# Optimization experiments

Measured on AMD Instinct MI355X. Metric: run time of the kernel, lower is better.

## Reference

```python
import jax, jax.numpy as jnp
import numpy as np

VOCAB, DIM, B, S = 32000, 1024, 64, 512

def setup_inputs() -> dict:
    key = jax.random.key(0)
    ks = jax.random.split(key, 16)
    std = 1.0 / np.sqrt(DIM)
    return {
        "x": jax.random.randint(ks[0], (B,), 0, VOCAB),
        "h": jax.random.normal(ks[1], (B, DIM), jnp.float32),
        "c": jax.random.normal(ks[2], (B, DIM), jnp.float32),
        "enc_y": jax.random.normal(ks[3], (B, S, DIM), jnp.float32),
        "F_emb": jax.random.normal(ks[4], (VOCAB, DIM), jnp.float32),
        "W1_w": jax.random.uniform(ks[5], (DIM, DIM), jnp.float32, -std, std),
        "W1_b": jnp.zeros((DIM,), jnp.float32),
        "W2_w": jax.random.uniform(ks[6], (DIM, DIM), jnp.float32, -std, std),
        "W2_b": jnp.zeros((DIM,), jnp.float32),
        "V_w": jax.random.uniform(ks[7], (1, DIM), jnp.float32, -std, std),
        "V_b": jnp.zeros((1,), jnp.float32),
        "W_ih": jax.random.uniform(ks[8], (4 * DIM, DIM), jnp.float32, -std, std),
        "W_hh": jax.random.uniform(ks[9], (4 * DIM, DIM), jnp.float32, -std, std),
        "b_ih": jax.random.uniform(ks[10], (4 * DIM,), jnp.float32, -std, std),
        "b_hh": jax.random.uniform(ks[11], (4 * DIM,), jnp.float32, -std, std),
        "fc_w": jax.random.uniform(ks[12], (VOCAB, DIM), jnp.float32, -std, std),
        "fc_b": jnp.zeros((VOCAB,), jnp.float32),
    }

def reference(x, h, c, enc_y, F_emb, W1_w, W1_b, W2_w, W2_b, V_w, V_b,
              W_ih, W_hh, b_ih, b_hh, fc_w, fc_b):
    # Bahdanau additive attention (weights returned; context is dead code for layer=1)
    i_s = jnp.einsum('bsd,ed->bse', enc_y, W1_w) + W1_b          # [B,S,D]
    j_s = (h @ W2_w.T + W2_b)[:, None, :]                        # [B,1,D]
    score = jnp.tanh(i_s + j_s)                                  # [B,S,D]
    att = jax.nn.softmax(score @ V_w.T + V_b, axis=1)            # [B,S,1]
    # embedding lookup for the step token
    emb = F_emb[x]                                               # [B,D]
    # single-step LSTM (pytorch gate order: i, f, g, o)
    gates = emb @ W_ih.T + b_ih + h @ W_hh.T + b_hh              # [B,4D]
    ig, fg, gg, og = jnp.split(gates, 4, axis=-1)
    c_new = jax.nn.sigmoid(fg) * c + jax.nn.sigmoid(ig) * jnp.tanh(gg)
    h_new = jax.nn.sigmoid(og) * jnp.tanh(c_new)
    out = h_new + emb                                            # residual skip
    logits = out @ fc_w.T + fc_b                                 # [B,VOCAB]
    return logits, h_new, c_new, att
```

## Files before the change

### kernel.cpp

```cpp
#include <hip/hip_runtime.h>

#define DEV __device__ __forceinline__

typedef __bf16 bf16_t;
typedef bf16_t bf16x8 __attribute__((ext_vector_type(8)));
typedef float f32x4 __attribute__((ext_vector_type(4)));

static constexpr int VOCAB = 32000, DIM = 1024, BATCH = 64, SEQ = 512;
static constexpr int M_SC = BATCH * SEQ;

DEV unsigned short f2bf(float f) {
  unsigned u = __builtin_bit_cast(unsigned, f);
  u += 0x7FFFu + ((u >> 16) & 1u);
  return (unsigned short)(u >> 16);
}

DEV float sigmf(float x) {
  x = fminf(fmaxf(x, -30.f), 30.f);
  return 1.0f / (1.0f + __expf(-x));
}

DEV float tanh_fast(float x) {
  x = fminf(fmaxf(x, -20.f), 20.f);
  float e = __expf(2.0f * x);
  return (e - 1.0f) / (e + 1.0f);
}

DEV void gload_lds16(const void* g, void* l) {
  __builtin_amdgcn_global_load_lds(
      (__attribute__((address_space(1))) void*)(g),
      (__attribute__((address_space(3))) void*)(l), 16, 0, 0);
}

__global__ void __launch_bounds__(256) k_prep(const float* __restrict__ enc,
                                              const float* __restrict__ w1,
                                              unsigned short* __restrict__ enc_b,
                                              unsigned short* __restrict__ w1_b,
                                              float* __restrict__ att_l,
                                              const int* __restrict__ x,
                                              const float* __restrict__ Femb,
                                              const float* __restrict__ h,
                                              float* __restrict__ emb_f,
                                              unsigned short* __restrict__ eh_b,
                                              unsigned short* __restrict__ h_b) {
  if (blockIdx.x >= 1984) {
    int b = blockIdx.x - 1984;
    int tok = x[b];
    for (int d = threadIdx.x; d < DIM; d += 256) {
      float e = Femb[(size_t)tok * DIM + d];
      float hv = h[b * DIM + d];
      emb_f[b * DIM + d] = e;
      unsigned short eb = f2bf(e), hb = f2bf(hv);
      eh_b[b * 2 * DIM + d] = eb;
      eh_b[b * 2 * DIM + DIM + d] = hb;
      h_b[b * DIM + d] = hb;
    }
  }
  int gid = blockIdx.x * 256 + threadIdx.x;
  if (gid < M_SC) att_l[gid] = 0.f;
  const int ENC4 = (M_SC * DIM) / 4;
  const int TOT4 = ENC4 + (DIM * DIM) / 4;
  int stride = gridDim.x * 256;
  for (int i = gid; i < TOT4; i += stride) {
    float4 v;
    unsigned short* dst;
    if (i < ENC4) {
      v = ((const float4*)enc)[i];
      dst = enc_b + (size_t)i * 4;
    } else {
      v = ((const float4*)w1)[i - ENC4];
      dst = w1_b + (size_t)(i - ENC4) * 4;
    }
    ushort4 o;
    o.x = f2bf(v.x); o.y = f2bf(v.y); o.z = f2bf(v.z); o.w = f2bf(v.w);
    *(ushort4*)dst = o;
  }
}

__global__ void __launch_bounds__(256) k_skinny(
    const unsigned short* __restrict__ A, int lda,
    const float* __restrict__ B1, const float* __restrict__ B2, int ksplit,
    const float* __restrict__ bias, float* __restrict__ C, int N, int K) {
  __shared__ unsigned short As[2][64 * 128];
  __shared__ unsigned short Bs[2][16 * 128];
  int t = threadIdx.x;
  int l = t & 63, w = t >> 6;
  int n0 = blockIdx.x * 16;
  f32x4 acc = {};
  int rx = (l & 7) << 3;

  float4 vB[2];

  auto loadB = [&](int k0) {
    const float* Bsrc;
    int kk;
    if (k0 < ksplit) { Bsrc = B1; kk = k0; } else { Bsrc = B2; kk = k0 - ksplit; }
#pragma unroll
    for (int i = 0; i < 2; ++i) {
      int lin = i * 256 + t;
      int row = lin >> 5, c4 = (lin & 31) * 4;
      vB[i] = *(const float4*)(Bsrc + (size_t)(n0 + row) * 1024 + kk + c4);
    }
  };
  auto writeB = [&](int bufi) {
#pragma unroll
    for (int i = 0; i < 2; ++i) {
      int lin = i * 256 + t;
      int row = lin >> 5, c4 = (lin & 31) * 4;
      ushort4 o;
      o.x = f2bf(vB[i].x); o.y = f2bf(vB[i].y); o.z = f2bf(vB[i].z); o.w = f2bf(vB[i].w);
      *(ushort4*)&Bs[bufi][row * 128 + (c4 ^ ((row & 7) << 3))] = o;
    }
  };
  auto stageA = [&](int k0, int bufi) {
#pragma unroll
    for (int i = 0; i < 4; ++i) {
      int sbase = i * 256 + w * 64;
      int s = sbase + l;
      int row = s >> 4;
      int scol = ((s & 15) ^ (row & 7)) * 8;
      gload_lds16(A + (size_t)row * lda + k0 + scol, &As[bufi][sbase * 8]);
    }
  };
  auto compute = [&](int bufi) {
#pragma unroll
    for (int kf = 0; kf < 4; ++kf) {
      int ko = kf * 32 + 8 * (l >> 4);
      int ar = w * 16 + (l & 15);
      bf16x8 af = *(const bf16x8*)&As[bufi][ar * 128 + (ko ^ rx)];
      bf16x8 bf = *(const bf16x8*)&Bs[bufi][(l & 15) * 128 + (ko ^ rx)];
      acc = __builtin_amdgcn_mfma_f32_16x16x32_bf16(af, bf, acc, 0, 0, 0);
    }
  };

  loadB(0);
  stageA(0, 0);
  writeB(0);
  asm volatile("s_waitcnt lgkmcnt(0)" ::: "memory");

  int nk = K / 128;
  int cur = 0;
  for (int kt = 0; kt < nk - 1; ++kt) {
    loadB((kt + 1) * 128);
    stageA((kt + 1) * 128, cur ^ 1);
    asm volatile("s_waitcnt vmcnt(6)\n\ts_barrier" ::: "memory");
    compute(cur);
    writeB(cur ^ 1);
    asm volatile("s_waitcnt lgkmcnt(0)\n\ts_barrier" ::: "memory");
    cur ^= 1;
  }
  asm volatile("s_waitcnt vmcnt(0)\n\ts_barrier" ::: "memory");
  compute(cur);

  int cn = n0 + (l & 15);
  float bv = bias ? bias[cn] : 0.f;
#pragma unroll
  for (int r = 0; r < 4; ++r) {
    int m = w * 16 + (l >> 4) * 4 + r;
    C[(size_t)m * N + cn] = acc[r] + bv;
  }
}

__global__ void __launch_bounds__(256) k_skinny32(
    const unsigned short* __restrict__ A,
    const float* __restrict__ B, const float* __restrict__ bias,
    float* __restrict__ C, int N, int K) {
  __shared__ unsigned short As[2][64 * 128];
  __shared__ unsigned short Bs[2][32 * 128];
  int t = threadIdx.x;
  int l = t & 63, w = t >> 6;
  int n0 = blockIdx.x * 32;
  f32x4 acc0 = {}, acc1 = {};
  int rx = (l & 7) << 3;

  float4 vB[4];

  auto loadB = [&](int k0) {
#pragma unroll
    for (int i = 0; i < 4; ++i) {
      int lin = i * 256 + t;
      int row = lin >> 5, c4 = (lin & 31) * 4;
      vB[i] = *(const float4*)(B + (size_t)(n0 + row) * 1024 + k0 + c4);
    }
  };
  auto writeB = [&](int bufi) {
#pragma unroll
    for (int i = 0; i < 4; ++i) {
      int lin = i * 256 + t;
      int row = lin >> 5, c4 = (lin & 31) * 4;
      ushort4 o;
      o.x = f2bf(vB[i].x); o.y = f2bf(vB[i].y); o.z = f2bf(vB[i].z); o.w = f2bf(vB[i].w);
      *(ushort4*)&Bs[bufi][row * 128 + (c4 ^ ((row & 7) << 3))] = o;
    }
  };
  auto stageA = [&](int k0, int bufi) {
#pragma unroll
    for (int i = 0; i < 4; ++i) {
      int sbase = i * 256 + w * 64;
      int s = sbase + l;
      int row = s >> 4;
      int scol = ((s & 15) ^ (row & 7)) * 8;
      gload_lds16(A + (size_t)row * DIM + k0 + scol, &As[bufi][sbase * 8]);
    }
  };
  auto compute = [&](int bufi) {
#pragma unroll
    for (int kf = 0; kf < 4; ++kf) {
      int ko = kf * 32 + 8 * (l >> 4);
      int ar = w * 16 + (l & 15);
      bf16x8 af = *(const bf16x8*)&As[bufi][ar * 128 + (ko ^ rx)];
      bf16x8 b0 = *(const bf16x8*)&Bs[bufi][(l & 15) * 128 + (ko ^ rx)];
      bf16x8 b1 = *(const bf16x8*)&Bs[bufi][((l & 15) + 16) * 128 + (ko ^ rx)];
      acc0 = __builtin_amdgcn_mfma_f32_16x16x32_bf16(af, b0, acc0, 0, 0, 0);
      acc1 = __builtin_amdgcn_mfma_f32_16x16x32_bf16(af, b1, acc1, 0, 0, 0);
    }
  };

  loadB(0);
  stageA(0, 0);
  writeB(0);
  asm volatile("s_waitcnt lgkmcnt(0)" ::: "memory");

  int nk = K / 128;
  int cur = 0;
  for (int kt = 0; kt < nk - 1; ++kt) {
    loadB((kt + 1) * 128);
    stageA((kt + 1) * 128, cur ^ 1);
    asm volatile("s_waitcnt vmcnt(8)\n\ts_barrier" ::: "memory");
    compute(cur);
    writeB(cur ^ 1);
    asm volatile("s_waitcnt lgkmcnt(0)\n\ts_barrier" ::: "memory");
    cur ^= 1;
  }
  asm volatile("s_waitcnt vmcnt(0)\n\ts_barrier" ::: "memory");
  compute(cur);

  int cn = n0 + (l & 15);
  float bv0 = bias ? bias[cn] : 0.f;
  float bv1 = bias ? bias[cn + 16] : 0.f;
#pragma unroll
  for (int r = 0; r < 4; ++r) {
    int m = w * 16 + (l >> 4) * 4 + r;
    C[(size_t)m * N + cn] = acc0[r] + bv0;
    C[(size_t)m * N + cn + 16] = acc1[r] + bv1;
  }
}

#define READ_A(MH)                                                              \
  do {                                                                          \
    _Pragma("unroll") for (int mf = 0; mf < 4; ++mf)                            \
    _Pragma("unroll") for (int kk = 0; kk < 2; ++kk) {                          \
      int row_ = wm * 128 + (MH) * 64 + mf * 16 + lm;                           \
      fa[mf][kk] = *(const bf16x8*)&As[ct][row_ * 64 + ((kk * 32 + 8 * lq) ^ rx)]; \
    }                                                                           \
  } while (0)
#define READ_B(NH)                                                              \
  do {                                                                          \
    _Pragma("unroll") for (int nf = 0; nf < 2; ++nf)                            \
    _Pragma("unroll") for (int kk = 0; kk < 2; ++kk) {                          \
      int row_ = wn * 64 + (NH) * 32 + nf * 16 + lm;                            \
      fb[NH][nf][kk] = *(const bf16x8*)&Bs[ct][row_ * 64 + ((kk * 32 + 8 * lq) ^ rx)]; \
    }                                                                           \
  } while (0)
#define MFMA_Q(MH, NH)                                                          \
  do {                                                                          \
    __builtin_amdgcn_s_setprio(1);                                              \
    _Pragma("unroll") for (int mf = 0; mf < 4; ++mf)                            \
    _Pragma("unroll") for (int nf = 0; nf < 2; ++nf)                            \
    _Pragma("unroll") for (int kk = 0; kk < 2; ++kk)                            \
        acc[(MH) * 4 + mf][(NH) * 2 + nf] = __builtin_amdgcn_mfma_f32_16x16x32_bf16( \
            fa[mf][kk], fb[NH][nf][kk], acc[(MH) * 4 + mf][(NH) * 2 + nf], 0, 0, 0); \
    __builtin_amdgcn_s_setprio(0);                                              \
  } while (0)

__global__ void __launch_bounds__(512, 2) k_score(
    const unsigned short* __restrict__ encb, const unsigned short* __restrict__ w1mat,
    const float* __restrict__ js, const float* __restrict__ w1bias,
    const float* __restrict__ vw, float* __restrict__ att_l) {
  __shared__ unsigned short As[2][256 * 64];
  __shared__ unsigned short Bs[2][256 * 64];
  int tid = threadIdx.x;
  int lane = tid & 63, wid = tid >> 6;
  int wm = wid >> 2, wn = wid & 3;
  int lm = lane & 15, lq = lane >> 4;
  int rx = (lane & 7) << 3;

  int wg = blockIdx.x;
  int swz = (wg & 7) * 64 + (wg >> 3);
  int m0 = (swz >> 2) * 256;
  int n0 = (swz & 3) * 256;

  const unsigned short* pa = encb + (size_t)m0 * DIM;
  const unsigned short* pb = w1mat + (size_t)n0 * DIM;

  f32x4 acc[8][4] = {};
  bf16x8 fa[4][2];
  bf16x8 fb[2][2][2];

  auto stageA = [&](int kt, int h, int bufi) {
#pragma unroll
    for (int i = 0; i < 2; ++i) {
      int rowbase = i * 128 + h * 64 + wid * 8;
      int row = rowbase + (lane >> 3);
      int scol = ((lane & 7) ^ (row & 7)) * 8;
      gload_lds16(pa + (size_t)row * DIM + kt * 64 + scol, &As[bufi][rowbase * 64]);
    }
  };
  auto stageB = [&](int kt, int h, int bufi) {
#pragma unroll
    for (int i = 0; i < 2; ++i) {
      int j0 = i * 64 + wid * 8;
      int rowbase = (j0 >> 5) * 64 + h * 32 + (j0 & 31);
      int row = rowbase + (lane >> 3);
      int scol = ((lane & 7) ^ (row & 7)) * 8;
      gload_lds16(pb + (size_t)row * DIM + kt * 64 + scol, &Bs[bufi][rowbase * 64]);
    }
  };

  stageA(0, 0, 0);
  stageB(0, 0, 0);
  stageB(0, 1, 0);
  stageA(0, 1, 0);
  asm volatile("s_waitcnt vmcnt(4)\n\ts_barrier" ::: "memory");

  for (int t = 0; t < 15; ++t) {
    const int ct = t & 1;
    READ_A(0); READ_B(0);
    stageA(t + 1, 0, ct ^ 1);
    asm volatile("s_waitcnt vmcnt(4)\n\ts_barrier" ::: "memory");
    MFMA_Q(0, 0);
    asm volatile("s_barrier" ::: "memory");
    READ_B(1);
    stageB(t + 1, 0, ct ^ 1);
    asm volatile("s_waitcnt vmcnt(4)\n\ts_barrier" ::: "memory");
    MFMA_Q(0, 1);
    asm volatile("s_barrier" ::: "memory");
    READ_A(1);
    stageB(t + 1, 1, ct ^ 1);
    asm volatile("s_barrier" ::: "memory");
    MFMA_Q(1, 1);
    asm volatile("s_barrier" ::: "memory");
    stageA(t + 1, 1, ct ^ 1);
    asm volatile("s_waitcnt vmcnt(4)\n\ts_barrier" ::: "memory");
    MFMA_Q(1, 0);
    asm volatile("s_barrier" ::: "memory");
  }
  {
    const int ct = 1;
    READ_A(0); READ_B(0);
    asm volatile("s_waitcnt vmcnt(2)\n\ts_barrier" ::: "memory");
    MFMA_Q(0, 0);
    asm volatile("s_barrier" ::: "memory");
    READ_B(1);
    asm volatile("s_waitcnt vmcnt(0)\n\ts_barrier" ::: "memory");
    MFMA_Q(0, 1);
    asm volatile("s_barrier" ::: "memory");
    READ_A(1);
    MFMA_Q(1, 1);
    MFMA_Q(1, 0);
  }

  int b = m0 >> 9;
  const float* jrow = js + b * DIM;
  float jvv[4], vvv[4];
#pragma unroll
  for (int nj = 0; nj < 4; ++nj) {
    int e = n0 + wn * 64 + nj * 16 + lm;
    jvv[nj] = jrow[e] + w1bias[e];
    vvv[nj] = vw[e];
  }
#pragma unroll
  for (int mi = 0; mi < 8; ++mi) {
    float psum[4] = {0.f, 0.f, 0.f, 0.f};
#pragma unroll
    for (int nj = 0; nj < 4; ++nj)
#pragma unroll
      for (int r = 0; r < 4; ++r)
        psum[r] += tanh_fast(acc[mi][nj][r] + jvv[nj]) * vvv[nj];
#pragma unroll
    for (int r = 0; r < 4; ++r) {
      float s = psum[r];
      s += __shfl_xor(s, 1);
      s += __shfl_xor(s, 2);
      s += __shfl_xor(s, 4);
      s += __shfl_xor(s, 8);
      if (lm == 0)
        atomicAdd(&att_l[m0 + wm * 128 + mi * 16 + lq * 4 + r], s);
    }
  }
}
#undef READ_A
#undef READ_B
#undef MFMA_Q

__global__ void k_softmax(const float* __restrict__ att_l, float* __restrict__ att) {
  __shared__ float red[16];
  int b = blockIdx.x, t = threadIdx.x;
  float v = att_l[b * SEQ + t];
  float m = v;
#pragma unroll
  for (int o = 32; o; o >>= 1) m = fmaxf(m, __shfl_xor(m, o));
  if ((t & 63) == 0) red[t >> 6] = m;
  __syncthreads();
  m = red[0];
#pragma unroll
  for (int i = 1; i < 8; ++i) m = fmaxf(m, red[i]);
  float e = __expf(v - m);
  float s = e;
#pragma unroll
  for (int o = 32; o; o >>= 1) s += __shfl_xor(s, o);
  __syncthreads();
  if ((t & 63) == 0) red[8 + (t >> 6)] = s;
  __syncthreads();
  s = 0.f;
#pragma unroll
  for (int i = 0; i < 8; ++i) s += red[8 + i];
  att[b * SEQ + t] = e / s;
}

__global__ void k_lstm(const float* __restrict__ gates, const float* __restrict__ bih,
                       const float* __restrict__ bhh, const float* __restrict__ c,
                       const float* __restrict__ emb_f, float* __restrict__ out_h,
                       float* __restrict__ out_c, unsigned short* __restrict__ out_b) {
  int t = blockIdx.x * 256 + threadIdx.x;
  int b = t >> 10, d = t & 1023;
  const float* g = gates + b * 4 * DIM;
  float ig = g[d] + bih[d] + bhh[d];
  float fg = g[DIM + d] + bih[DIM + d] + bhh[DIM + d];
  float gg = g[2 * DIM + d] + bih[2 * DIM + d] + bhh[2 * DIM + d];
  float og = g[3 * DIM + d] + bih[3 * DIM + d] + bhh[3 * DIM + d];
  float cn = sigmf(fg) * c[t] + sigmf(ig) * tanh_fast(gg);
  float hn = sigmf(og) * tanh_fast(cn);
  out_h[t] = hn;
  out_c[t] = cn;
  out_b[t] = f2bf(hn + emb_f[t]);
}

extern "C" void kernel_launch(void* const* d_in, const int* in_sizes, int n_in,
                              void* d_out, int out_size, void* d_ws, size_t ws_size,
                              hipStream_t stream) {
  const int* x = (const int*)d_in[0];
  const float* h = (const float*)d_in[1];
  const float* c = (const float*)d_in[2];
  const float* enc = (const float*)d_in[3];
  const float* Femb = (const float*)d_in[4];
  const float* W1w = (const float*)d_in[5];
  const float* W1b = (const float*)d_in[6];
  const float* W2w = (const float*)d_in[7];
  const float* W2b = (const float*)d_in[8];
  const float* Vw = (const float*)d_in[9];
  const float* Wih = (const float*)d_in[11];
  const float* Whh = (const float*)d_in[12];
  const float* bih = (const float*)d_in[13];
  const float* bhh = (const float*)d_in[14];
  const float* fcw = (const float*)d_in[15];
  const float* fcb = (const float*)d_in[16];

  float* out_logits = (float*)d_out;
  float* out_h = out_logits + (size_t)BATCH * VOCAB;
  float* out_c = out_h + BATCH * DIM;
  float* out_att = out_c + BATCH * DIM;

  char* p = (char*)d_ws;
  unsigned short* enc_b = (unsigned short*)p; p += (size_t)M_SC * DIM * 2;
  unsigned short* w1_b = (unsigned short*)p;  p += (size_t)DIM * DIM * 2;
  float* att_l = (float*)p;                   p += (size_t)M_SC * 4;
  float* js = (float*)p;                      p += (size_t)BATCH * DIM * 4;
  float* emb_f = (float*)p;                   p += (size_t)BATCH * DIM * 4;
  unsigned short* eh_b = (unsigned short*)p;  p += (size_t)BATCH * 2 * DIM * 2;
  unsigned short* h_b = (unsigned short*)p;   p += (size_t)BATCH * DIM * 2;
  float* gates = (float*)p;                   p += (size_t)BATCH * 4 * DIM * 4;
  unsigned short* out_b = (unsigned short*)p; p += (size_t)BATCH * DIM * 2;

  hipLaunchKernelGGL(k_prep, dim3(2048), dim3(256), 0, stream, enc, W1w, enc_b, w1_b,
                     att_l, x, Femb, h, emb_f, eh_b, h_b);
  hipLaunchKernelGGL(k_skinny, dim3(DIM / 16), dim3(256), 0, stream,
                     h_b, DIM, W2w, W2w, DIM, W2b, js, DIM, DIM);
  hipLaunchKernelGGL(k_score, dim3(512), dim3(512), 0, stream,
                     enc_b, w1_b, js, W1b, Vw, att_l);
  hipLaunchKernelGGL(k_softmax, dim3(BATCH), dim3(SEQ), 0, stream, att_l, out_att);
  hipLaunchKernelGGL(k_skinny, dim3(4 * DIM / 16), dim3(256), 0, stream,
                     eh_b, 2 * DIM, Wih, Whh, DIM, (const float*)nullptr, gates, 4 * DIM, 2 * DIM);
  hipLaunchKernelGGL(k_lstm, dim3(BATCH * DIM / 256), dim3(256), 0, stream,
                     gates, bih, bhh, c, emb_f, out_h, out_c, out_b);
  hipLaunchKernelGGL(k_skinny32, dim3(VOCAB / 32), dim3(256), 0, stream,
                     out_b, fcw, fcb, out_logits, VOCAB, DIM);
}
```

Before: 180.9 us.

## Process two N tiles per score block in one continuous K pipeline

```diff
diff --git a/kernel.cpp b/kernel.cpp
--- a/kernel.cpp
+++ b/kernel.cpp
@@ -286,12 +286,24 @@
   int rx = (lane & 7) << 3;
 
   int wg = blockIdx.x;
-  int swz = (wg & 7) * 64 + (wg >> 3);
-  int m0 = (swz >> 2) * 256;
-  int n0 = (swz & 3) * 256;
+  int swz = (wg & 7) * 32 + (wg >> 3);
+  int m0 = (swz >> 1) * 256;
+  int n0b = (swz & 1) * 512;
 
   const unsigned short* pa = encb + (size_t)m0 * DIM;
-  const unsigned short* pb = w1mat + (size_t)n0 * DIM;
+  const unsigned short* pb0 = w1mat + (size_t)n0b * DIM;
+  const unsigned short* pb1 = w1mat + (size_t)(n0b + 256) * DIM;
+
+  int bb = m0 >> 9;
+  float jvv[2][4], vvv[2][4];
+#pragma unroll
+  for (int rp = 0; rp < 2; ++rp)
+#pragma unroll
+    for (int nj = 0; nj < 4; ++nj) {
+      int e = n0b + rp * 256 + wn * 64 + nj * 16 + lm;
+      jvv[rp][nj] = js[bb * DIM + e] + w1bias[e];
+      vvv[rp][nj] = vw[e];
+    }
 
   f32x4 acc[8][4] = {};
   bf16x8 fa[4][2];
@@ -306,44 +318,75 @@
       gload_lds16(pa + (size_t)row * DIM + kt * 64 + scol, &As[bufi][rowbase * 64]);
     }
   };
-  auto stageB = [&](int kt, int h, int bufi) {
+  auto stageB = [&](const unsigned short* pbx, int kt, int h, int bufi) {
 #pragma unroll
     for (int i = 0; i < 2; ++i) {
       int j0 = i * 64 + wid * 8;
       int rowbase = (j0 >> 5) * 64 + h * 32 + (j0 & 31);
       int row = rowbase + (lane >> 3);
       int scol = ((lane & 7) ^ (row & 7)) * 8;
-      gload_lds16(pb + (size_t)row * DIM + kt * 64 + scol, &Bs[bufi][rowbase * 64]);
+      gload_lds16(pbx + (size_t)row * DIM + kt * 64 + scol, &Bs[bufi][rowbase * 64]);
+    }
+  };
+  auto epilogue = [&](int rp) {
+#pragma unroll
+    for (int mi = 0; mi < 8; ++mi) {
+      float psum[4] = {0.f, 0.f, 0.f, 0.f};
+#pragma unroll
+      for (int nj = 0; nj < 4; ++nj)
+#pragma unroll
+        for (int r = 0; r < 4; ++r)
+          psum[r] += tanh_fast(acc[mi][nj][r] + jvv[rp][nj]) * vvv[rp][nj];
+#pragma unroll
+      for (int r = 0; r < 4; ++r) {
+        float s = psum[r];
+        s += __shfl_xor(s, 1);
+        s += __shfl_xor(s, 2);
+        s += __shfl_xor(s, 4);
+        s += __shfl_xor(s, 8);
+        if (lm == 0)
+          atomicAdd(&att_l[m0 + wm * 128 + mi * 16 + lq * 4 + r], s);
+      }
     }
   };
 
   stageA(0, 0, 0);
-  stageB(0, 0, 0);
-  stageB(0, 1, 0);
+  stageB(pb0, 0, 0, 0);
+  stageB(pb0, 0, 1, 0);
   stageA(0, 1, 0);
   asm volatile("s_waitcnt vmcnt(4)\n\ts_barrier" ::: "memory");
 
-  for (int t = 0; t < 15; ++t) {
+  for (int t = 0; t < 31; ++t) {
     const int ct = t & 1;
+    const int nkt = (t + 1) & 15;
+    const unsigned short* pbn = ((t + 1) >> 4) ? pb1 : pb0;
     READ_A(0); READ_B(0);
-    stageA(t + 1, 0, ct ^ 1);
+    stageA(nkt, 0, ct ^ 1);
     asm volatile("s_waitcnt vmcnt(4)\n\ts_barrier" ::: "memory");
     MFMA_Q(0, 0);
     asm volatile("s_barrier" ::: "memory");
     READ_B(1);
-    stageB(t + 1, 0, ct ^ 1);
+    stageB(pbn, nkt, 0, ct ^ 1);
     asm volatile("s_waitcnt vmcnt(4)\n\ts_barrier" ::: "memory");
     MFMA_Q(0, 1);
     asm volatile("s_barrier" ::: "memory");
     READ_A(1);
-    stageB(t + 1, 1, ct ^ 1);
+    stageB(pbn, nkt, 1, ct ^ 1);
     asm volatile("s_barrier" ::: "memory");
     MFMA_Q(1, 1);
     asm volatile("s_barrier" ::: "memory");
-    stageA(t + 1, 1, ct ^ 1);
+    stageA(nkt, 1, ct ^ 1);
     asm volatile("s_waitcnt vmcnt(4)\n\ts_barrier" ::: "memory");
     MFMA_Q(1, 0);
     asm volatile("s_barrier" ::: "memory");
+    if (t == 15) {
+      epilogue(0);
+#pragma unroll
+      for (int i = 0; i < 8; ++i)
+#pragma unroll
+        for (int j = 0; j < 4; ++j)
+          acc[i][j] = f32x4{0.f, 0.f, 0.f, 0.f};
+    }
   }
   {
     const int ct = 1;
@@ -359,35 +402,7 @@
     MFMA_Q(1, 1);
     MFMA_Q(1, 0);
   }
-
-  int b = m0 >> 9;
-  const float* jrow = js + b * DIM;
-  float jvv[4], vvv[4];
-#pragma unroll
-  for (int nj = 0; nj < 4; ++nj) {
-    int e = n0 + wn * 64 + nj * 16 + lm;
-    jvv[nj] = jrow[e] + w1bias[e];
-    vvv[nj] = vw[e];
-  }
-#pragma unroll
-  for (int mi = 0; mi < 8; ++mi) {
-    float psum[4] = {0.f, 0.f, 0.f, 0.f};
-#pragma unroll
-    for (int nj = 0; nj < 4; ++nj)
-#pragma unroll
-      for (int r = 0; r < 4; ++r)
-        psum[r] += tanh_fast(acc[mi][nj][r] + jvv[nj]) * vvv[nj];
-#pragma unroll
-    for (int r = 0; r < 4; ++r) {
-      float s = psum[r];
-      s += __shfl_xor(s, 1);
-      s += __shfl_xor(s, 2);
-      s += __shfl_xor(s, 4);
-      s += __shfl_xor(s, 8);
-      if (lm == 0)
-        atomicAdd(&att_l[m0 + wm * 128 + mi * 16 + lq * 4 + r], s);
-    }
-  }
+  epilogue(1);
 }
 #undef READ_A
 #undef READ_B
@@ -476,7 +491,7 @@
                      att_l, x, Femb, h, emb_f, eh_b, h_b);
   hipLaunchKernelGGL(k_skinny, dim3(DIM / 16), dim3(256), 0, stream,
                      h_b, DIM, W2w, W2w, DIM, W2b, js, DIM, DIM);
-  hipLaunchKernelGGL(k_score, dim3(512), dim3(512), 0, stream,
+  hipLaunchKernelGGL(k_score, dim3(256), dim3(512), 0, stream,
                      enc_b, w1_b, js, W1b, Vw, att_l);
   hipLaunchKernelGGL(k_softmax, dim3(BATCH), dim3(SEQ), 0, stream, att_l, out_att);
   hipLaunchKernelGGL(k_skinny, dim3(4 * DIM / 16), dim3(256), 0, stream,
```

Result: slower. 195.7 us (+8.2%).

## Fuse encoder fp32-to-bf16 conversion into score GEMM A-tile staging

Applied to the files above, without the earlier changes.

```diff
diff --git a/kernel.cpp b/kernel.cpp
--- a/kernel.cpp
+++ b/kernel.cpp
@@ -32,19 +32,17 @@
       (__attribute__((address_space(3))) void*)(l), 16, 0, 0);
 }
 
-__global__ void __launch_bounds__(256) k_prep(const float* __restrict__ enc,
-                                              const float* __restrict__ w1,
-                                              unsigned short* __restrict__ enc_b,
-                                              unsigned short* __restrict__ w1_b,
-                                              float* __restrict__ att_l,
-                                              const int* __restrict__ x,
-                                              const float* __restrict__ Femb,
-                                              const float* __restrict__ h,
-                                              float* __restrict__ emb_f,
-                                              unsigned short* __restrict__ eh_b,
-                                              unsigned short* __restrict__ h_b) {
-  if (blockIdx.x >= 1984) {
-    int b = blockIdx.x - 1984;
+__global__ void __launch_bounds__(256) k_small(const float* __restrict__ w1,
+                                               unsigned short* __restrict__ w1_b,
+                                               float* __restrict__ att_l,
+                                               const int* __restrict__ x,
+                                               const float* __restrict__ Femb,
+                                               const float* __restrict__ h,
+                                               float* __restrict__ emb_f,
+                                               unsigned short* __restrict__ eh_b,
+                                               unsigned short* __restrict__ h_b) {
+  if (blockIdx.x >= 960) {
+    int b = blockIdx.x - 960;
     int tok = x[b];
     for (int d = threadIdx.x; d < DIM; d += 256) {
       float e = Femb[(size_t)tok * DIM + d];
@@ -58,23 +56,10 @@
   }
   int gid = blockIdx.x * 256 + threadIdx.x;
   if (gid < M_SC) att_l[gid] = 0.f;
-  const int ENC4 = (M_SC * DIM) / 4;
-  const int TOT4 = ENC4 + (DIM * DIM) / 4;
-  int stride = gridDim.x * 256;
-  for (int i = gid; i < TOT4; i += stride) {
-    float4 v;
-    unsigned short* dst;
-    if (i < ENC4) {
-      v = ((const float4*)enc)[i];
-      dst = enc_b + (size_t)i * 4;
-    } else {
-      v = ((const float4*)w1)[i - ENC4];
-      dst = w1_b + (size_t)(i - ENC4) * 4;
-    }
-    ushort4 o;
-    o.x = f2bf(v.x); o.y = f2bf(v.y); o.z = f2bf(v.z); o.w = f2bf(v.w);
-    *(ushort4*)dst = o;
-  }
+  float4 v = ((const float4*)w1)[gid];
+  ushort4 o;
+  o.x = f2bf(v.x); o.y = f2bf(v.y); o.z = f2bf(v.z); o.w = f2bf(v.w);
+  *(ushort4*)(w1_b + (size_t)gid * 4) = o;
 }
 
 __global__ void __launch_bounds__(256) k_skinny(
@@ -273,8 +258,8 @@
     __builtin_amdgcn_s_setprio(0);                                              \
   } while (0)
 
-__global__ void __launch_bounds__(512, 2) k_score(
-    const unsigned short* __restrict__ encb, const unsigned short* __restrict__ w1mat,
+__global__ void __launch_bounds__(512, 1) k_score(
+    const float* __restrict__ enc, const unsigned short* __restrict__ w1mat,
     const float* __restrict__ js, const float* __restrict__ w1bias,
     const float* __restrict__ vw, float* __restrict__ att_l) {
   __shared__ unsigned short As[2][256 * 64];
@@ -290,21 +275,45 @@
   int m0 = (swz >> 2) * 256;
   int n0 = (swz & 3) * 256;
 
-  const unsigned short* pa = encb + (size_t)m0 * DIM;
+  const float* pa = enc + (size_t)m0 * DIM;
   const unsigned short* pb = w1mat + (size_t)n0 * DIM;
 
   f32x4 acc[8][4] = {};
   bf16x8 fa[4][2];
   bf16x8 fb[2][2][2];
 
-  auto stageA = [&](int kt, int h, int bufi) {
-#pragma unroll
-    for (int i = 0; i < 2; ++i) {
-      int rowbase = i * 128 + h * 64 + wid * 8;
-      int row = rowbase + (lane >> 3);
-      int scol = ((lane & 7) ^ (row & 7)) * 8;
-      gload_lds16(pa + (size_t)row * DIM + kt * 64 + scol, &As[bufi][rowbase * 64]);
-    }
+  int ar4 = tid >> 2;
+  int ac = (tid & 3) * 16;
+  int grE = (ar4 & 63) + ((ar4 >> 6) << 7);
+  float4 vAE[4], vAO[4];
+
+  auto loadE = [&](int kt) {
+    const float* s = pa + (size_t)grE * DIM + kt * 64 + ac;
+#pragma unroll
+    for (int q = 0; q < 4; ++q) vAE[q] = *(const float4*)(s + q * 4);
+  };
+  auto loadO = [&](int kt) {
+    const float* s = pa + (size_t)(grE + 64) * DIM + kt * 64 + ac;
+#pragma unroll
+    for (int q = 0; q < 4; ++q) vAO[q] = *(const float4*)(s + q * 4);
+  };
+  auto packw = [&](float4 a, float4 b, unsigned short* dst) {
+    uint4 o;
+    o.x = (unsigned)f2bf(a.x) | ((unsigned)f2bf(a.y) << 16);
+    o.y = (unsigned)f2bf(a.z) | ((unsigned)f2bf(a.w) << 16);
+    o.z = (unsigned)f2bf(b.x) | ((unsigned)f2bf(b.y) << 16);
+    o.w = (unsigned)f2bf(b.z) | ((unsigned)f2bf(b.w) << 16);
+    *(uint4*)dst = o;
+  };
+  auto writeE = [&](int bufi) {
+    int gr = grE, base = gr * 64, c8 = (tid & 3) * 2, xr = (gr & 7);
+    packw(vAE[0], vAE[1], &As[bufi][base + ((c8 ^ xr) << 3)]);
+    packw(vAE[2], vAE[3], &As[bufi][base + (((c8 + 1) ^ xr) << 3)]);
+  };
+  auto writeO = [&](int bufi) {
+    int gr = grE + 64, base = gr * 64, c8 = (tid & 3) * 2, xr = (gr & 7);
+    packw(vAO[0], vAO[1], &As[bufi][base + ((c8 ^ xr) << 3)]);
+    packw(vAO[2], vAO[3], &As[bufi][base + (((c8 + 1) ^ xr) << 3)]);
   };
   auto stageB = [&](int kt, int h, int bufi) {
 #pragma unroll
@@ -317,42 +326,47 @@
     }
   };
 
-  stageA(0, 0, 0);
+  loadE(0);
+  loadO(0);
   stageB(0, 0, 0);
   stageB(0, 1, 0);
-  stageA(0, 1, 0);
-  asm volatile("s_waitcnt vmcnt(4)\n\ts_barrier" ::: "memory");
+  writeE(0);
+  writeO(0);
+  asm volatile("s_waitcnt vmcnt(2)" ::: "memory");
+  asm volatile("s_waitcnt lgkmcnt(0)\n\ts_barrier" ::: "memory");
 
   for (int t = 0; t < 15; ++t) {
     const int ct = t & 1;
     READ_A(0); READ_B(0);
-    stageA(t + 1, 0, ct ^ 1);
-    asm volatile("s_waitcnt vmcnt(4)\n\ts_barrier" ::: "memory");
+    loadE(t + 1);
+    stageB(t + 1, 0, ct ^ 1);
+    asm volatile("s_waitcnt vmcnt(6)\n\ts_barrier" ::: "memory");
     MFMA_Q(0, 0);
     asm volatile("s_barrier" ::: "memory");
     READ_B(1);
-    stageB(t + 1, 0, ct ^ 1);
-    asm volatile("s_waitcnt vmcnt(4)\n\ts_barrier" ::: "memory");
+    loadO(t + 1);
+    stageB(t + 1, 1, ct ^ 1);
+    asm volatile("s_barrier" ::: "memory");
     MFMA_Q(0, 1);
     asm volatile("s_barrier" ::: "memory");
     READ_A(1);
-    stageB(t + 1, 1, ct ^ 1);
-    asm volatile("s_barrier" ::: "memory");
+    writeE(ct ^ 1);
+    asm volatile("s_waitcnt lgkmcnt(0)\n\ts_barrier" ::: "memory");
     MFMA_Q(1, 1);
     asm volatile("s_barrier" ::: "memory");
-    stageA(t + 1, 1, ct ^ 1);
-    asm volatile("s_waitcnt vmcnt(4)\n\ts_barrier" ::: "memory");
+    writeO(ct ^ 1);
+    asm volatile("s_waitcnt lgkmcnt(0)\n\ts_barrier" ::: "memory");
     MFMA_Q(1, 0);
     asm volatile("s_barrier" ::: "memory");
   }
   {
     const int ct = 1;
     READ_A(0); READ_B(0);
-    asm volatile("s_waitcnt vmcnt(2)\n\ts_barrier" ::: "memory");
+    asm volatile("s_waitcnt vmcnt(0)\n\ts_barrier" ::: "memory");
     MFMA_Q(0, 0);
     asm volatile("s_barrier" ::: "memory");
     READ_B(1);
-    asm volatile("s_waitcnt vmcnt(0)\n\ts_barrier" ::: "memory");
+    asm volatile("s_barrier" ::: "memory");
     MFMA_Q(0, 1);
     asm volatile("s_barrier" ::: "memory");
     READ_A(1);
@@ -462,7 +476,6 @@
   float* out_att = out_c + BATCH * DIM;
 
   char* p = (char*)d_ws;
-  unsigned short* enc_b = (unsigned short*)p; p += (size_t)M_SC * DIM * 2;
   unsigned short* w1_b = (unsigned short*)p;  p += (size_t)DIM * DIM * 2;
   float* att_l = (float*)p;                   p += (size_t)M_SC * 4;
   float* js = (float*)p;                      p += (size_t)BATCH * DIM * 4;
@@ -472,12 +485,12 @@
   float* gates = (float*)p;                   p += (size_t)BATCH * 4 * DIM * 4;
   unsigned short* out_b = (unsigned short*)p; p += (size_t)BATCH * DIM * 2;
 
-  hipLaunchKernelGGL(k_prep, dim3(2048), dim3(256), 0, stream, enc, W1w, enc_b, w1_b,
-                     att_l, x, Femb, h, emb_f, eh_b, h_b);
+  hipLaunchKernelGGL(k_small, dim3(1024), dim3(256), 0, stream,
+                     W1w, w1_b, att_l, x, Femb, h, emb_f, eh_b, h_b);
   hipLaunchKernelGGL(k_skinny, dim3(DIM / 16), dim3(256), 0, stream,
                      h_b, DIM, W2w, W2w, DIM, W2b, js, DIM, DIM);
   hipLaunchKernelGGL(k_score, dim3(512), dim3(512), 0, stream,
-                     enc_b, w1_b, js, W1b, Vw, att_l);
+                     enc, w1_b, js, W1b, Vw, att_l);
   hipLaunchKernelGGL(k_softmax, dim3(BATCH), dim3(SEQ), 0, stream, att_l, out_att);
   hipLaunchKernelGGL(k_skinny, dim3(4 * DIM / 16), dim3(256), 0, stream,
                      eh_b, 2 * DIM, Wih, Whh, DIM, (const float*)nullptr, gates, 4 * DIM, 2 * DIM);
```

Measured after the change: 220.8 us. +22.0%, slower.
